# Kernel optimization log

Measured on AMD Instinct MI355X. Metric: run time of the kernel, lower is better.

Reference implementation:

```python
import jax, jax.numpy as jnp
import numpy as np

B, S, H = 8, 4096, 1024
N_IDX = 65536
N_SEG = 8192


def setup_inputs() -> dict:
    key = jax.random.key(0)
    k1, k2, k3, k4, k5 = jax.random.split(key, 5)
    transformer_hidden = jax.random.normal(k1, (B, S, H), dtype=jnp.float32)
    indices = jax.random.randint(k2, (N_IDX,), 0, B * S, dtype=jnp.int32)
    segment_ids = jnp.sort(jax.random.randint(k3, (N_IDX,), 0, N_SEG, dtype=jnp.int32))
    W_dense = jax.random.normal(k4, (H, H), dtype=jnp.float32) * (1.0 / np.sqrt(H))
    b_dense = jnp.zeros((H,), dtype=jnp.float32)
    W_proj = jax.random.normal(k5, (1, H), dtype=jnp.float32) * (1.0 / np.sqrt(H))
    b_proj = jnp.zeros((1,), dtype=jnp.float32)
    return {
        "transformer_hidden": transformer_hidden,
        "indices": indices,
        "segment_ids": segment_ids,
        "W_dense": W_dense,
        "b_dense": b_dense,
        "W_proj": W_proj,
        "b_proj": b_proj,
    }


def reference(transformer_hidden, indices, segment_ids, W_dense, b_dense, W_proj, b_proj):
    # Flatten tokens: [B*S, H]
    hid = transformer_hidden.reshape(-1, transformer_hidden.shape[-1])
    # Ragged gather of grouped token indices, then per-group mean (segment mean)
    gathered = hid[indices]  # [n_idx, H]
    sums = jax.ops.segment_sum(gathered, segment_ids, num_segments=N_SEG)  # [G, H]
    counts = jax.ops.segment_sum(
        jnp.ones((indices.shape[0],), dtype=hid.dtype), segment_ids, num_segments=N_SEG
    )
    h = sums / jnp.maximum(counts, 1.0)[:, None]  # [G, H] group means
    # dense -> gelu (torch exact erf gelu) -> lin_proj -> flatten
    z = jax.nn.gelu(h @ W_dense.T + b_dense, approximate=False)
    predictions = z @ W_proj.T + b_proj  # [G, 1]
    return predictions.reshape(-1)
```

## Files before the change

kernel.cpp:

```cpp
#include <hip/hip_runtime.h>
#include <stdint.h>

#define BH   (8 * 4096)
#define HDIM 1024
#define NIDX 65536
#define NSEG 8192
#define KD   1024
#define ND   1024

typedef __bf16 bf16x8 __attribute__((ext_vector_type(8)));
typedef float  f32x4  __attribute__((ext_vector_type(4)));

__device__ __forceinline__ unsigned short f2bf(float f) {
  unsigned int u = __float_as_uint(f);
  u += 0x7fffu + ((u >> 16) & 1u);
  return (unsigned short)(u >> 16);
}

__device__ __forceinline__ void async16(const void* g, void* l) {
  __builtin_amdgcn_global_load_lds(
      (const __attribute__((address_space(1))) void*)g,
      (__attribute__((address_space(3))) void*)l,
      16, 0, 0);
}

__global__ void convw_kernel(const float* __restrict__ W, unsigned short* __restrict__ Wb) {
  int i = (blockIdx.x * 256 + threadIdx.x) * 4;
  float4 v = *(const float4*)(W + i);
  ushort4 o;
  o.x = f2bf(v.x); o.y = f2bf(v.y); o.z = f2bf(v.z); o.w = f2bf(v.w);
  *(ushort4*)(Wb + i) = o;
}

__global__ void bounds_kernel(const int* __restrict__ seg, int* __restrict__ starts) {
  int i = blockIdx.x * 256 + threadIdx.x;
  if (i > NIDX) return;
  int prev = (i == 0) ? -1 : seg[i - 1];
  int cur  = (i == NIDX) ? NSEG : seg[i];
  for (int g = prev + 1; g <= cur; ++g) starts[g] = i;
}

__global__ void segmean_kernel(const float* __restrict__ hid,
                               const int* __restrict__ indices,
                               const int* __restrict__ starts,
                               unsigned short* __restrict__ hb,
                               float* __restrict__ out,
                               const float* __restrict__ b_proj) {
  const int g = blockIdx.x;
  const int t = threadIdx.x;
  const int start = starts[g];
  const int end   = starts[g + 1];

  float4 acc = make_float4(0.f, 0.f, 0.f, 0.f);
  for (int i = start; i < end; ++i) {
    int r = indices[i];
    float4 v = *(const float4*)(hid + (size_t)r * HDIM + t * 4);
    acc.x += v.x; acc.y += v.y; acc.z += v.z; acc.w += v.w;
  }
  const float inv = 1.0f / fmaxf((float)(end - start), 1.0f);
  ushort4 o;
  o.x = f2bf(acc.x * inv); o.y = f2bf(acc.y * inv);
  o.z = f2bf(acc.z * inv); o.w = f2bf(acc.w * inv);
  *(ushort4*)(hb + (size_t)g * HDIM + t * 4) = o;

  if (t == 0) out[g] = b_proj[0];
}

__global__ void __launch_bounds__(256)
gemm_gelu_proj_kernel(const unsigned short* __restrict__ A,
                      const unsigned short* __restrict__ Bw,
                      const float* __restrict__ b_dense,
                      const float* __restrict__ w_proj,
                      float* __restrict__ out) {
  __shared__ alignas(16) unsigned short As[128 * 32];
  __shared__ alignas(16) unsigned short Bs[64 * 32];

  const int tid  = threadIdx.x;
  const int lane = tid & 63;
  const int wave = tid >> 6;
  const int wm   = wave >> 1;
  const int wn   = wave & 1;
  const int m0   = blockIdx.x * 128;
  const int n0   = blockIdx.y * 64;
  const int lr   = lane & 15;
  const int quad = lane >> 4;

  f32x4 acc[4][2];
#pragma unroll
  for (int mi = 0; mi < 4; ++mi)
#pragma unroll
    for (int ni = 0; ni < 2; ++ni) {
      acc[mi][ni][0] = 0.f; acc[mi][ni][1] = 0.f;
      acc[mi][ni][2] = 0.f; acc[mi][ni][3] = 0.f;
    }

  for (int kt = 0; kt < KD / 32; ++kt) {
    const int k0 = kt * 32;
#pragma unroll
    for (int j = 0; j < 2; ++j) {
      int c   = j * 256 + wave * 64 + lane;
      int row = c >> 2, sl = c & 3;
      int kcg = sl ^ ((row >> 1) & 3);
      async16(A + (size_t)(m0 + row) * KD + k0 + kcg * 8,
              (char*)As + (j * 256 + wave * 64) * 16);
    }
    {
      int c   = wave * 64 + lane;
      int row = c >> 2, sl = c & 3;
      int kcg = sl ^ ((row >> 1) & 3);
      async16(Bw + (size_t)(n0 + row) * KD + k0 + kcg * 8,
              (char*)Bs + (wave * 64) * 16);
    }
    __syncthreads();

    bf16x8 af[4], bf_[2];
#pragma unroll
    for (int i = 0; i < 4; ++i) {
      int ra  = wm * 64 + i * 16 + lr;
      int sla = quad ^ ((ra >> 1) & 3);
      af[i] = *(const bf16x8*)(As + ra * 32 + sla * 8);
    }
#pragma unroll
    for (int i = 0; i < 2; ++i) {
      int rb  = wn * 32 + i * 16 + lr;
      int slb = quad ^ ((rb >> 1) & 3);
      bf_[i] = *(const bf16x8*)(Bs + rb * 32 + slb * 8);
    }
#pragma unroll
    for (int mi = 0; mi < 4; ++mi)
#pragma unroll
      for (int ni = 0; ni < 2; ++ni)
        acc[mi][ni] = __builtin_amdgcn_mfma_f32_16x16x32_bf16(af[mi], bf_[ni], acc[mi][ni], 0, 0, 0);
    __syncthreads();
  }

#pragma unroll
  for (int mi = 0; mi < 4; ++mi) {
    float rp[4] = {0.f, 0.f, 0.f, 0.f};
#pragma unroll
    for (int ni = 0; ni < 2; ++ni) {
      int col  = n0 + wn * 32 + ni * 16 + lr;
      float bd = b_dense[col];
      float wp = w_proj[col];
#pragma unroll
      for (int r = 0; r < 4; ++r) {
        float v  = acc[mi][ni][r] + bd;
        float gl = 0.5f * v * (1.0f + erff(v * 0.70710678118654752f));
        rp[r] += gl * wp;
      }
    }
#pragma unroll
    for (int r = 0; r < 4; ++r) {
      float c = rp[r];
      c += __shfl_xor(c, 1);
      c += __shfl_xor(c, 2);
      c += __shfl_xor(c, 4);
      c += __shfl_xor(c, 8);
      if (lr == 0)
        atomicAdd(out + (m0 + wm * 64 + mi * 16 + quad * 4 + r), c);
    }
  }
}

extern "C" void kernel_launch(void* const* d_in, const int* in_sizes, int n_in,
                              void* d_out, int out_size, void* d_ws, size_t ws_size,
                              hipStream_t stream) {
  const float* hid     = (const float*)d_in[0];
  const int*   indices = (const int*)d_in[1];
  const int*   seg     = (const int*)d_in[2];
  const float* W_dense = (const float*)d_in[3];
  const float* b_dense = (const float*)d_in[4];
  const float* W_proj  = (const float*)d_in[5];
  const float* b_proj  = (const float*)d_in[6];
  float* out = (float*)d_out;

  unsigned short* hb     = (unsigned short*)d_ws;
  unsigned short* Wb     = (unsigned short*)((char*)d_ws + (size_t)NSEG * KD * 2);
  int*            starts = (int*)((char*)d_ws + (size_t)NSEG * KD * 2 + (size_t)ND * KD * 2);

  convw_kernel<<<dim3((ND * KD) / 1024), 256, 0, stream>>>(W_dense, Wb);
  bounds_kernel<<<dim3((NIDX + 256) / 256), 256, 0, stream>>>(seg, starts);
  segmean_kernel<<<dim3(NSEG), 256, 0, stream>>>(hid, indices, starts, hb, out, b_proj);
  gemm_gelu_proj_kernel<<<dim3(NSEG / 128, ND / 64), 256, 0, stream>>>(hb, Wb, b_dense, W_proj, out);
}
```

Baseline: 243.6 us.

## Replace LDS-staged GEMM with per-wave direct-register loads and double buffering

The GEMM kernel no longer stages A and B tiles through shared memory with block-wide barriers. Each wave now owns its own 64x64 output tile and loads its bf16 fragments straight from global memory into registers, double-buffering two K-steps so the loads overlap the MFMAs. This removes LDS traffic and __syncthreads, but it also drops data reuse between waves, so every wave reads its own A and B rows through the caches, and it raises register pressure with a 4x4 accumulator array plus four fragment buffers.

```diff
diff --git a/kernel.cpp b/kernel.cpp
--- a/kernel.cpp
+++ b/kernel.cpp
@@ -15,13 +15,6 @@
   unsigned int u = __float_as_uint(f);
   u += 0x7fffu + ((u >> 16) & 1u);
   return (unsigned short)(u >> 16);
-}
-
-__device__ __forceinline__ void async16(const void* g, void* l) {
-  __builtin_amdgcn_global_load_lds(
-      (const __attribute__((address_space(1))) void*)g,
-      (__attribute__((address_space(3))) void*)l,
-      16, 0, 0);
 }
 
 __global__ void convw_kernel(const float* __restrict__ W, unsigned short* __restrict__ Wb) {
@@ -72,74 +65,73 @@
                       const float* __restrict__ b_dense,
                       const float* __restrict__ w_proj,
                       float* __restrict__ out) {
-  __shared__ alignas(16) unsigned short As[128 * 32];
-  __shared__ alignas(16) unsigned short Bs[64 * 32];
-
   const int tid  = threadIdx.x;
   const int lane = tid & 63;
   const int wave = tid >> 6;
-  const int wm   = wave >> 1;
-  const int wn   = wave & 1;
-  const int m0   = blockIdx.x * 128;
-  const int n0   = blockIdx.y * 64;
+  const int w    = blockIdx.x * 4 + wave;
+  const int mt   = w >> 4;
+  const int nt   = w & 15;
   const int lr   = lane & 15;
   const int quad = lane >> 4;
 
-  f32x4 acc[4][2];
+  const unsigned short* pA[4];
+  const unsigned short* pB[4];
+#pragma unroll
+  for (int i = 0; i < 4; ++i) {
+    pA[i] = A  + (size_t)(mt * 64 + i * 16 + lr) * KD + quad * 8;
+    pB[i] = Bw + (size_t)(nt * 64 + i * 16 + lr) * KD + quad * 8;
+  }
+
+  f32x4 acc[4][4];
 #pragma unroll
   for (int mi = 0; mi < 4; ++mi)
 #pragma unroll
-    for (int ni = 0; ni < 2; ++ni) {
+    for (int ni = 0; ni < 4; ++ni) {
       acc[mi][ni][0] = 0.f; acc[mi][ni][1] = 0.f;
       acc[mi][ni][2] = 0.f; acc[mi][ni][3] = 0.f;
     }
 
-  for (int kt = 0; kt < KD / 32; ++kt) {
-    const int k0 = kt * 32;
+  bf16x8 a0[4], b0[4], a1[4], b1[4];
 #pragma unroll
-    for (int j = 0; j < 2; ++j) {
-      int c   = j * 256 + wave * 64 + lane;
-      int row = c >> 2, sl = c & 3;
-      int kcg = sl ^ ((row >> 1) & 3);
-      async16(A + (size_t)(m0 + row) * KD + k0 + kcg * 8,
-              (char*)As + (j * 256 + wave * 64) * 16);
-    }
-    {
-      int c   = wave * 64 + lane;
-      int row = c >> 2, sl = c & 3;
-      int kcg = sl ^ ((row >> 1) & 3);
-      async16(Bw + (size_t)(n0 + row) * KD + k0 + kcg * 8,
-              (char*)Bs + (wave * 64) * 16);
-    }
-    __syncthreads();
+  for (int i = 0; i < 4; ++i) {
+    a0[i] = *(const bf16x8*)(pA[i]);
+    b0[i] = *(const bf16x8*)(pB[i]);
+  }
 
-    bf16x8 af[4], bf_[2];
+#pragma unroll 1
+  for (int kt = 0; kt < 16; ++kt) {
 #pragma unroll
     for (int i = 0; i < 4; ++i) {
-      int ra  = wm * 64 + i * 16 + lr;
-      int sla = quad ^ ((ra >> 1) & 3);
-      af[i] = *(const bf16x8*)(As + ra * 32 + sla * 8);
-    }
-#pragma unroll
-    for (int i = 0; i < 2; ++i) {
-      int rb  = wn * 32 + i * 16 + lr;
-      int slb = quad ^ ((rb >> 1) & 3);
-      bf_[i] = *(const bf16x8*)(Bs + rb * 32 + slb * 8);
+      a1[i] = *(const bf16x8*)(pA[i] + 32);
+      b1[i] = *(const bf16x8*)(pB[i] + 32);
     }
 #pragma unroll
     for (int mi = 0; mi < 4; ++mi)
 #pragma unroll
-      for (int ni = 0; ni < 2; ++ni)
-        acc[mi][ni] = __builtin_amdgcn_mfma_f32_16x16x32_bf16(af[mi], bf_[ni], acc[mi][ni], 0, 0, 0);
-    __syncthreads();
+      for (int ni = 0; ni < 4; ++ni)
+        acc[mi][ni] = __builtin_amdgcn_mfma_f32_16x16x32_bf16(a0[mi], b0[ni], acc[mi][ni], 0, 0, 0);
+    if (kt != 15) {
+#pragma unroll
+      for (int i = 0; i < 4; ++i) {
+        a0[i] = *(const bf16x8*)(pA[i] + 64);
+        b0[i] = *(const bf16x8*)(pB[i] + 64);
+      }
+    }
+#pragma unroll
+    for (int mi = 0; mi < 4; ++mi)
+#pragma unroll
+      for (int ni = 0; ni < 4; ++ni)
+        acc[mi][ni] = __builtin_amdgcn_mfma_f32_16x16x32_bf16(a1[mi], b1[ni], acc[mi][ni], 0, 0, 0);
+#pragma unroll
+    for (int i = 0; i < 4; ++i) { pA[i] += 64; pB[i] += 64; }
   }
 
 #pragma unroll
   for (int mi = 0; mi < 4; ++mi) {
     float rp[4] = {0.f, 0.f, 0.f, 0.f};
 #pragma unroll
-    for (int ni = 0; ni < 2; ++ni) {
-      int col  = n0 + wn * 32 + ni * 16 + lr;
+    for (int ni = 0; ni < 4; ++ni) {
+      int col  = nt * 64 + ni * 16 + lr;
       float bd = b_dense[col];
       float wp = w_proj[col];
 #pragma unroll
@@ -157,7 +149,7 @@
       c += __shfl_xor(c, 4);
       c += __shfl_xor(c, 8);
       if (lr == 0)
-        atomicAdd(out + (m0 + wm * 64 + mi * 16 + quad * 4 + r), c);
+        atomicAdd(out + (mt * 64 + mi * 16 + quad * 4 + r), c);
     }
   }
 }
@@ -181,5 +173,5 @@
   convw_kernel<<<dim3((ND * KD) / 1024), 256, 0, stream>>>(W_dense, Wb);
   bounds_kernel<<<dim3((NIDX + 256) / 256), 256, 0, stream>>>(seg, starts);
   segmean_kernel<<<dim3(NSEG), 256, 0, stream>>>(hid, indices, starts, hb, out, b_proj);
-  gemm_gelu_proj_kernel<<<dim3(NSEG / 128, ND / 64), 256, 0, stream>>>(hb, Wb, b_dense, W_proj, out);
+  gemm_gelu_proj_kernel<<<dim3((NSEG / 64) * (ND / 64) / 4), 256, 0, stream>>>(hb, Wb, b_dense, W_proj, out);
 }
```

After: 280.6 us. +15.2%, slower.
